# Kernel tuning notes

Measured on AMD Instinct MI355X. Metric: run time of the kernel, lower is better.

## Reference

```python
import jax, jax.numpy as jnp
import numpy as np

HEAD_DIM = 1024
SCALE = HEAD_DIM ** -0.25  # qk_scale defaults to exponent -0.25


def setup_inputs() -> dict:
    key = jax.random.key(0)
    ks = jax.random.split(key, 6)
    B_s, B_q, C = 4096, 4096, 1024
    return {
        "query": jax.random.normal(ks[0], (B_q, C), dtype=jnp.float32),
        "s": jax.random.normal(ks[1], (B_s, C), dtype=jnp.float32),
        "TG_prompt": jax.random.normal(ks[2], (B_s, C), dtype=jnp.float32),
        "W_qkv": jax.random.normal(ks[3], (3 * HEAD_DIM, C), dtype=jnp.float32) * (C ** -0.5),
        "W_proj_s": jax.random.normal(ks[4], (HEAD_DIM, HEAD_DIM), dtype=jnp.float32) * (HEAD_DIM ** -0.5),
        "W_proj_q": jax.random.normal(ks[5], (HEAD_DIM, HEAD_DIM), dtype=jnp.float32) * (HEAD_DIM ** -0.5),
    }


def reference(query, s, TG_prompt, W_qkv, W_proj_s, W_proj_q):
    B_s = s.shape[0]
    t = s + TG_prompt                       # [B_s, C]
    c = jnp.concatenate([t, query], axis=0)  # [B, C], B = B_s + B_q
    x = c @ W_qkv.T                          # [B, 3*head_dim]
    q, k, v = jnp.split(x, 3, axis=-1)       # each [B, head_dim]
    # separate sqrt-scale on q and k, then full [B, B] scores
    attn = jax.nn.softmax((q * SCALE) @ (k.T * SCALE), axis=-1)
    attn_cq = attn[:B_s, B_s:]               # [B_s, B_q]
    attn_qc = attn[B_s:, :B_s]               # [B_q, B_s]
    # matmul against raw query / s (NOT v), then per-branch projection
    x_s = (attn_cq @ query) @ W_proj_s.T     # [B_s, head_dim]
    x_q = (attn_qc @ s) @ W_proj_q.T         # [B_q, head_dim]
    return (x_s, x_q)
```

## Files before the change

### kernel.cpp

```cpp
#include <hip/hip_runtime.h>


typedef unsigned short u16;
typedef __bf16 bf16x8 __attribute__((ext_vector_type(8)));
typedef float f32x4 __attribute__((ext_vector_type(4)));
typedef unsigned short u16x8 __attribute__((ext_vector_type(8)));

#define DEVI static __device__ __forceinline__

DEVI u16 f2b(float f) {
  unsigned int u = __float_as_uint(f);
  u += 0x7fffu + ((u >> 16) & 1u);
  return (u16)(u >> 16);
}

DEVI float exp2_hw(float x) {
  float r;
  asm("v_exp_f32 %0, %1" : "=v"(r) : "v"(x));
  return r;
}

__global__ void prep_all(const float* __restrict__ query, const float* __restrict__ s,
                         const float* __restrict__ tg, const float* __restrict__ w0,
                         const float* __restrict__ w1, const float* __restrict__ w2,
                         u16* __restrict__ cB, u16* __restrict__ sBf,
                         u16* __restrict__ o0, u16* __restrict__ o1,
                         u16* __restrict__ o2, float* __restrict__ rowsum) {
  int b = blockIdx.x;
  if (b >= 6144) {
    int i = (b - 6144) * 1024 + (int)threadIdx.x * 4;
    rowsum[i] = 0.f; rowsum[i + 1] = 0.f; rowsum[i + 2] = 0.f; rowsum[i + 3] = 0.f;
    return;
  }
  if (b < 4096) {
    int base = (b * 256 + threadIdx.x) << 3;
    int row = base >> 10;
    u16x8 o;
    if (row < 4096) {
      float4 a0 = *(const float4*)(s + base);
      float4 a1 = *(const float4*)(s + base + 4);
      float4 b0 = *(const float4*)(tg + base);
      float4 b1 = *(const float4*)(tg + base + 4);
      u16x8 os;
      os[0] = f2b(a0.x); os[1] = f2b(a0.y); os[2] = f2b(a0.z); os[3] = f2b(a0.w);
      os[4] = f2b(a1.x); os[5] = f2b(a1.y); os[6] = f2b(a1.z); os[7] = f2b(a1.w);
      *(u16x8*)(sBf + base) = os;
      o[0] = f2b(a0.x + b0.x); o[1] = f2b(a0.y + b0.y);
      o[2] = f2b(a0.z + b0.z); o[3] = f2b(a0.w + b0.w);
      o[4] = f2b(a1.x + b1.x); o[5] = f2b(a1.y + b1.y);
      o[6] = f2b(a1.z + b1.z); o[7] = f2b(a1.w + b1.w);
    } else {
      int qb = base - 4096 * 1024;
      float4 a0 = *(const float4*)(query + qb);
      float4 a1 = *(const float4*)(query + qb + 4);
      o[0] = f2b(a0.x); o[1] = f2b(a0.y); o[2] = f2b(a0.z); o[3] = f2b(a0.w);
      o[4] = f2b(a1.x); o[5] = f2b(a1.y); o[6] = f2b(a1.z); o[7] = f2b(a1.w);
    }
    *(u16x8*)(cB + base) = o;
  } else {
    const float* in; u16* out; int lb;
    if (b < 5120)      { in = w0; out = o0; lb = b - 4096; }
    else if (b < 5632) { in = w1; out = o1; lb = b - 5120; }
    else               { in = w2; out = o2; lb = b - 5632; }
    int base = (lb * 256 + threadIdx.x) << 3;
    float4 a0 = *(const float4*)(in + base);
    float4 a1 = *(const float4*)(in + base + 4);
    u16x8 o;
    o[0] = f2b(a0.x); o[1] = f2b(a0.y); o[2] = f2b(a0.z); o[3] = f2b(a0.w);
    o[4] = f2b(a1.x); o[5] = f2b(a1.y); o[6] = f2b(a1.z); o[7] = f2b(a1.w);
    *(u16x8*)(out + base) = o;
  }
}

DEVI void kloop(const u16* Ab, const u16* Bb, int lda, int ldb, int K,
                u16* sA, u16* sB, int tid, int wr, int wc, f32x4 (&acc)[4][4]) {
  const int lane = tid & 63;
  const int ar = lane & 15;
  const int sr = tid >> 3;
  const int scL = (tid & 7) << 3;
  const int scG = ((tid & 7) ^ (sr & 7)) << 3;

  const int l7 = lane & 7, l16 = lane >> 4;
  const int p0b = (l16 ^ l7) << 4;
  const int offA0 = (wr + ar) * 128 + p0b;
  const int offB0 = (wc + ar) * 128 + p0b;
  const char* sAc = (const char*)sA;
  const char* sBc = (const char*)sB;

  for (int k0 = 0; k0 < K; k0 += 64) {
#pragma unroll
    for (int it = 0; it < 4; ++it) {
      int r = it * 64 + sr;
      __builtin_amdgcn_global_load_lds(
          (__attribute__((address_space(1))) void*)(Ab + (size_t)r * lda + k0 + scG),
          (__attribute__((address_space(3))) void*)(sA + r * 64 + scL), 16, 0, 0);
    }
#pragma unroll
    for (int it = 0; it < 2; ++it) {
      int r = it * 64 + sr;
      __builtin_amdgcn_global_load_lds(
          (__attribute__((address_space(1))) void*)(Bb + (size_t)r * ldb + k0 + scG),
          (__attribute__((address_space(3))) void*)(sB + r * 64 + scL), 16, 0, 0);
    }
    __syncthreads();
#pragma unroll
    for (int half = 0; half < 2; ++half) {
      const int px = half ? 64 : 0;
      bf16x8 af[4], bfr[4];
#pragma unroll
      for (int t = 0; t < 4; ++t)
        af[t] = *(const bf16x8*)(sAc + ((offA0 ^ px) + t * 2048));
#pragma unroll
      for (int t = 0; t < 4; ++t)
        bfr[t] = *(const bf16x8*)(sBc + ((offB0 ^ px) + t * 2048));
#pragma unroll
      for (int tm = 0; tm < 4; ++tm)
#pragma unroll
        for (int tn = 0; tn < 4; ++tn)
          acc[tm][tn] = __builtin_amdgcn_mfma_f32_16x16x32_bf16(
              af[tm], bfr[tn], acc[tm][tn], 0, 0, 0);
    }
    __syncthreads();
  }
}

__global__ __launch_bounds__(512)
void gemm_qkv(const u16* __restrict__ cB, const u16* __restrict__ WqkB,
              u16* __restrict__ qks,
              const u16* __restrict__ WpsB, const u16* __restrict__ WpqB,
              const u16* __restrict__ qBf, const u16* __restrict__ sBf,
              u16* __restrict__ VsT, u16* __restrict__ VqT,
              float sq, float sk) {
  __shared__ __align__(16) u16 sA[256 * 64];
  __shared__ __align__(16) u16 sB[128 * 64];
  const int b = blockIdx.x;
  const u16* Ap; const u16* Bp; u16* op;
  int bx, by, ldc;
  bool proj;
  if (b < 512) {
    proj = true;  bx = b & 15; by = b >> 4;
    Ap = cB; Bp = WqkB; op = qks; ldc = 2048;
  } else {
    proj = false;
    int b2 = b - 512;
    int z = b2 >> 7, rem = b2 & 127;
    bx = rem & 31; by = rem >> 5;
    Ap = z ? WpqB : WpsB; Bp = z ? sBf : qBf; op = z ? VqT : VsT; ldc = 4096;
  }
  const int tid = threadIdx.x;
  const int lane = tid & 63;
  const int wave = tid >> 6;
  const int wr = (wave >> 1) * 64;
  const int wc = (wave & 1) * 64;

  f32x4 acc[4][4];
#pragma unroll
  for (int i = 0; i < 4; ++i)
#pragma unroll
    for (int j = 0; j < 4; ++j) acc[i][j] = f32x4{0.f, 0.f, 0.f, 0.f};

  kloop(Ap + (size_t)(by * 256) * 1024, Bp + (size_t)(bx * 128) * 1024,
        1024, 1024, 1024, sA, sB, tid, wr, wc, acc);

  const int qr = (lane >> 4) * 4;
  const int qc = lane & 15;
#pragma unroll
  for (int tm = 0; tm < 4; ++tm)
#pragma unroll
    for (int r = 0; r < 4; ++r) {
      int row = by * 256 + wr + tm * 16 + qr + r;
#pragma unroll
      for (int tn = 0; tn < 4; ++tn) {
        int col = bx * 128 + wc + tn * 16 + qc;
        float sc = proj ? ((col < 1024) ? sq : sk) : 1.0f;
        op[(size_t)row * ldc + col] = f2b(acc[tm][tn][r] * sc);
      }
    }
}

__global__ __launch_bounds__(512)
void gemm_sc(const u16* __restrict__ A, const u16* __restrict__ B,
             u16* __restrict__ Pcq, u16* __restrict__ Pqc,
             float* __restrict__ rowsum) {
  __shared__ __align__(16) u16 lds[2][2][256 * 64];
  const int tid = threadIdx.x;
  const int lane = tid & 63;
  const int wave = tid >> 6;
  const int wm = wave >> 2;
  const int wn = wave & 3;
  const int bx = blockIdx.x, by = blockIdx.y;

  const int sr = tid >> 3;
  const int scL = (tid & 7) << 3;
  const int scG = ((tid & 7) ^ (sr & 7)) << 3;

  const int l7 = lane & 7, l16 = lane >> 4;
  const int ar = lane & 15;
  const int p0b = (l16 ^ l7) << 4;
  const int offA0 = (wm * 128 + ar) * 128 + p0b;
  const int offB0 = (wn * 64 + ar) * 128 + p0b;

  const u16* Ag = A + (size_t)(by * 256) * 2048;
  const u16* Bg = B + (size_t)(bx * 256) * 2048;

#define STAGE_SC(DST, K0)                                                     \
  _Pragma("unroll")                                                           \
  for (int it_ = 0; it_ < 4; ++it_) {                                         \
    const int r_ = it_ * 64 + sr;                                             \
    __builtin_amdgcn_global_load_lds(                                         \
        (__attribute__((address_space(1))) void*)(Ag + (size_t)r_ * 2048 + (K0) + scG), \
        (__attribute__((address_space(3))) void*)(&lds[DST][0][r_ * 64 + scL]), 16, 0, 0); \
    __builtin_amdgcn_global_load_lds(                                         \
        (__attribute__((address_space(1))) void*)(Bg + (size_t)r_ * 2048 + (K0) + scG), \
        (__attribute__((address_space(3))) void*)(&lds[DST][1][r_ * 64 + scL]), 16, 0, 0); \
  }

#define MFMA_Q(MQ, NQ)                                                        \
  _Pragma("unroll")                                                           \
  for (int tm_ = 0; tm_ < 4; ++tm_) {                                         \
    _Pragma("unroll")                                                         \
    for (int tn_ = 0; tn_ < 2; ++tn_) {                                       \
      _Pragma("unroll")                                                       \
      for (int kh_ = 0; kh_ < 2; ++kh_)                                       \
        acc[(MQ) * 4 + tm_][(NQ) * 2 + tn_] =                                 \
            __builtin_amdgcn_mfma_f32_16x16x32_bf16(                          \
                af[tm_][kh_], bfr[NQ][tn_][kh_],                              \
                acc[(MQ) * 4 + tm_][(NQ) * 2 + tn_], 0, 0, 0);                \
    }                                                                         \
  }

  f32x4 acc[8][4];
#pragma unroll
  for (int i = 0; i < 8; ++i)
#pragma unroll
    for (int j = 0; j < 4; ++j) acc[i][j] = f32x4{0.f, 0.f, 0.f, 0.f};

  STAGE_SC(0, 0)

#pragma unroll 1
  for (int kt = 0; kt < 16; ++kt) {
    const int cur = kt & 1;
    const char* sAc = (const char*)lds[cur][0];
    const char* sBc = (const char*)lds[cur][1];

    if (kt < 15) {
      STAGE_SC(cur ^ 1, (kt + 1) * 64)
      asm volatile("s_waitcnt vmcnt(8)\n\ts_barrier" ::: "memory");
    } else {
      asm volatile("s_waitcnt vmcnt(0)\n\ts_barrier" ::: "memory");
    }

    bf16x8 af[4][2];
    bf16x8 bfr[2][2][2];
#pragma unroll
    for (int t_ = 0; t_ < 4; ++t_) {
      af[t_][0] = *(const bf16x8*)(sAc + (offA0 + t_ * 2048));
      af[t_][1] = *(const bf16x8*)(sAc + ((offA0 + t_ * 2048) ^ 64));
    }
#pragma unroll
    for (int nq_ = 0; nq_ < 2; ++nq_)
#pragma unroll
      for (int t_ = 0; t_ < 2; ++t_) {
        bfr[nq_][t_][0] = *(const bf16x8*)(sBc + (offB0 + nq_ * 4096 + t_ * 2048));
        bfr[nq_][t_][1] = *(const bf16x8*)(sBc + ((offB0 + nq_ * 4096 + t_ * 2048) ^ 64));
      }
    asm volatile("s_waitcnt lgkmcnt(0)" ::: "memory");
    __builtin_amdgcn_sched_barrier(0);
    __builtin_amdgcn_s_setprio(1);
    MFMA_Q(0, 0)
    __builtin_amdgcn_s_setprio(0);
    asm volatile("s_barrier" ::: "memory");

    __builtin_amdgcn_s_setprio(1);
    MFMA_Q(0, 1)
    __builtin_amdgcn_s_setprio(0);
    asm volatile("s_barrier" ::: "memory");

#pragma unroll
    for (int t_ = 0; t_ < 4; ++t_) {
      af[t_][0] = *(const bf16x8*)(sAc + (offA0 + 8192 + t_ * 2048));
      af[t_][1] = *(const bf16x8*)(sAc + ((offA0 + 8192 + t_ * 2048) ^ 64));
    }
    asm volatile("s_waitcnt lgkmcnt(0)" ::: "memory");
    __builtin_amdgcn_sched_barrier(0);
    __builtin_amdgcn_s_setprio(1);
    MFMA_Q(1, 0)
    __builtin_amdgcn_s_setprio(0);
    asm volatile("s_barrier" ::: "memory");

    __builtin_amdgcn_s_setprio(1);
    MFMA_Q(1, 1)
    __builtin_amdgcn_s_setprio(0);
    asm volatile("s_barrier" ::: "memory");
  }

  const int qr = (lane >> 4) * 4;
  const int qc = lane & 15;
  const bool top = (by < 16);
  const bool left = (bx < 16);
  u16* pdst = nullptr;
  if (top && !left) pdst = Pcq;
  if (!top && left) pdst = Pqc;
  const int growb = by * 256 + wm * 128;
  const int rbase = growb - (top ? 0 : 4096);
  const int cbase = bx * 256 + wn * 64 - (left ? 0 : 4096);
#pragma unroll
  for (int i = 0; i < 8; ++i) {
    float e[4][4];
    float rsum[4] = {0.f, 0.f, 0.f, 0.f};
#pragma unroll
    for (int j = 0; j < 4; ++j)
#pragma unroll
      for (int r = 0; r < 4; ++r) {
        e[j][r] = exp2_hw(acc[i][j][r]);
        rsum[r] += e[j][r];
      }
#pragma unroll
    for (int r = 0; r < 4; ++r) {
      float v = rsum[r];
      v += __shfl_xor(v, 1);
      v += __shfl_xor(v, 2);
      v += __shfl_xor(v, 4);
      v += __shfl_xor(v, 8);
      if ((lane & 15) == 0)
        atomicAdd(&rowsum[growb + i * 16 + qr + r], v);
    }
    if (pdst) {
#pragma unroll
      for (int j = 0; j < 4; ++j)
#pragma unroll
        for (int r = 0; r < 4; ++r) {
          int row = rbase + i * 16 + qr + r;
          pdst[(size_t)row * 4096 + cbase + j * 16 + qc] = f2b(e[j][r]);
        }
    }
  }
#undef STAGE_SC
#undef MFMA_Q
}

template <int EPI>
__global__ __launch_bounds__(512)
void gemm_bt(const u16* __restrict__ A, const u16* __restrict__ A1,
             const u16* __restrict__ B, const u16* __restrict__ B1,
             int lda, int ldb, int K, int ldc,
             float* __restrict__ outf, float* __restrict__ outf1,
             const float* __restrict__ rs, const float* __restrict__ rs1,
             u16* __restrict__ Pcq, u16* __restrict__ Pqc,
             float* __restrict__ rowsum) {
  __shared__ __align__(16) u16 sA[256 * 64];
  __shared__ __align__(16) u16 sB[128 * 64];
  const int tid = threadIdx.x;
  const int lane = tid & 63;
  const int wave = tid >> 6;
  const int wr = (wave >> 1) * 64;
  const int wc = (wave & 1) * 64;
  const int by = blockIdx.y, bx = blockIdx.x;
  const int z = blockIdx.z;

  f32x4 acc[4][4];
#pragma unroll
  for (int i = 0; i < 4; ++i)
#pragma unroll
    for (int j = 0; j < 4; ++j) acc[i][j] = f32x4{0.f, 0.f, 0.f, 0.f};

  kloop((z ? A1 : A) + (size_t)(by * 256) * lda,
        (z ? B1 : B) + (size_t)(bx * 128) * ldb,
        lda, ldb, K, sA, sB, tid, wr, wc, acc);

  const int qr = (lane >> 4) * 4;
  const int qc = lane & 15;

  if constexpr (EPI == 4) {
    float* of = z ? outf1 : outf;
    const float* rsz = z ? rs1 : rs;
#pragma unroll
    for (int tm = 0; tm < 4; ++tm)
#pragma unroll
      for (int r = 0; r < 4; ++r) {
        int row = by * 256 + wr + tm * 16 + qr + r;
        float inv = 1.0f / rsz[row];
#pragma unroll
        for (int tn = 0; tn < 4; ++tn) {
          int col = bx * 128 + wc + tn * 16 + qc;
          of[(size_t)row * ldc + col] = acc[tm][tn][r] * inv;
        }
      }
  }
}


extern "C" void kernel_launch(void* const* d_in, const int* in_sizes, int n_in,
                              void* d_out, int out_size, void* d_ws, size_t ws_size,
                              hipStream_t stream) {
  (void)in_sizes; (void)n_in; (void)out_size; (void)ws_size;
  const float* query = (const float*)d_in[0];
  const float* s     = (const float*)d_in[1];
  const float* tg    = (const float*)d_in[2];
  const float* Wqkv  = (const float*)d_in[3];
  const float* Wps   = (const float*)d_in[4];
  const float* Wpq   = (const float*)d_in[5];
  float* out = (float*)d_out;

  char* ws = (char*)d_ws;
  u16* cB     = (u16*)ws; ws += (size_t)8192 * 1024 * 2;
  u16* sBf    = (u16*)ws; ws += (size_t)4096 * 1024 * 2;
  u16* qks    = (u16*)ws; ws += (size_t)8192 * 2048 * 2;
  u16* WqkB   = (u16*)ws; ws += (size_t)2048 * 1024 * 2;
  u16* WpsB   = (u16*)ws; ws += (size_t)1024 * 1024 * 2;
  u16* WpqB   = (u16*)ws; ws += (size_t)1024 * 1024 * 2;
  u16* VsT    = (u16*)ws; ws += (size_t)1024 * 4096 * 2;
  u16* VqT    = (u16*)ws; ws += (size_t)1024 * 4096 * 2;
  u16* Pcq    = (u16*)ws; ws += (size_t)4096 * 4096 * 2;
  u16* Pqc    = (u16*)ws; ws += (size_t)4096 * 4096 * 2;
  float* rowsum = (float*)ws;

  const u16* qBf = cB + (size_t)4096 * 1024;

  const float SCALE = 0.17677669529663687f;
  const float LOG2E = 1.4426950408889634f;

  prep_all<<<6152, 256, 0, stream>>>(query, s, tg, Wqkv, Wps, Wpq,
                                     cB, sBf, WqkB, WpsB, WpqB, rowsum);
  gemm_qkv<<<768, 512, 0, stream>>>(cB, WqkB, qks, WpsB, WpqB, qBf, sBf,
                                    VsT, VqT, SCALE * LOG2E, SCALE);
  gemm_sc<<<dim3(32, 32), 512, 0, stream>>>(qks, qks + 1024, Pcq, Pqc, rowsum);
  gemm_bt<4><<<dim3(8, 16, 2), 512, 0, stream>>>(
      Pcq, Pqc, VsT, VqT, 4096, 4096, 4096, 1024,
      out, out + (size_t)4096 * 1024, rowsum, rowsum + 4096,
      nullptr, nullptr, nullptr);
}
```

Before: 448.0 us.

## Deepen score GEMM pipeline to two-stage-ahead prefetch with staggered A/B reloads

Reworks the K loop of the score GEMM so the global-to-LDS loads for tile kt+2 are issued into the buffer being consumed, split into B and A halves. Each half is issued right after its last LDS read completes, instead of prefetching only one tile ahead at the top of the loop. Fragment loads are split into af0/af1/b0/b1 groups interleaved with the MFMA quarters, and the explicit lgkmcnt waits, sched barriers and one s_barrier per iteration are removed. The aim is to hide more global-load latency and cut synchronisation stalls. In exchange the buffer-reuse ordering becomes more fragile, and register pressure from extra fragment arrays may rise.

New measurement: 452.9 us. About the same (+1.1%).

```diff
diff --git a/kernel.cpp b/kernel.cpp
--- a/kernel.cpp
+++ b/kernel.cpp
@@ -203,29 +203,26 @@
   const u16* Ag = A + (size_t)(by * 256) * 2048;
   const u16* Bg = B + (size_t)(bx * 256) * 2048;
 
-#define STAGE_SC(DST, K0)                                                     \
+#define STG(BUF, MAT, HALF, K0, SRC)                                          \
   _Pragma("unroll")                                                           \
-  for (int it_ = 0; it_ < 4; ++it_) {                                         \
-    const int r_ = it_ * 64 + sr;                                             \
+  for (int l_ = 0; l_ < 2; ++l_) {                                            \
+    const int r_ = (HALF) * 128 + l_ * 64 + sr;                               \
     __builtin_amdgcn_global_load_lds(                                         \
-        (__attribute__((address_space(1))) void*)(Ag + (size_t)r_ * 2048 + (K0) + scG), \
-        (__attribute__((address_space(3))) void*)(&lds[DST][0][r_ * 64 + scL]), 16, 0, 0); \
-    __builtin_amdgcn_global_load_lds(                                         \
-        (__attribute__((address_space(1))) void*)(Bg + (size_t)r_ * 2048 + (K0) + scG), \
-        (__attribute__((address_space(3))) void*)(&lds[DST][1][r_ * 64 + scL]), 16, 0, 0); \
-  }
-
-#define MFMA_Q(MQ, NQ)                                                        \
+        (__attribute__((address_space(1))) void*)((SRC) + (size_t)r_ * 2048 + (K0) + scG), \
+        (__attribute__((address_space(3))) void*)(&lds[BUF][MAT][r_ * 64 + scL]), 16, 0, 0); \
+  }
+
+#define MFMA_Q(AF, BF, MB, NB)                                                \
   _Pragma("unroll")                                                           \
   for (int tm_ = 0; tm_ < 4; ++tm_) {                                         \
     _Pragma("unroll")                                                         \
     for (int tn_ = 0; tn_ < 2; ++tn_) {                                       \
       _Pragma("unroll")                                                       \
       for (int kh_ = 0; kh_ < 2; ++kh_)                                       \
-        acc[(MQ) * 4 + tm_][(NQ) * 2 + tn_] =                                 \
+        acc[(MB) + tm_][(NB) + tn_] =                                         \
             __builtin_amdgcn_mfma_f32_16x16x32_bf16(                          \
-                af[tm_][kh_], bfr[NQ][tn_][kh_],                              \
-                acc[(MQ) * 4 + tm_][(NQ) * 2 + tn_], 0, 0, 0);                \
+                AF[tm_][kh_], BF[tn_][kh_], acc[(MB) + tm_][(NB) + tn_],      \
+                0, 0, 0);                                                     \
     }                                                                         \
   }
 
@@ -235,7 +232,10 @@
 #pragma unroll
     for (int j = 0; j < 4; ++j) acc[i][j] = f32x4{0.f, 0.f, 0.f, 0.f};
 
-  STAGE_SC(0, 0)
+  STG(0, 0, 0, 0, Ag) STG(0, 0, 1, 0, Ag)
+  STG(0, 1, 0, 0, Bg) STG(0, 1, 1, 0, Bg)
+  STG(1, 0, 0, 64, Ag) STG(1, 0, 1, 64, Ag)
+  STG(1, 1, 0, 64, Bg) STG(1, 1, 1, 64, Bg)
 
 #pragma unroll 1
   for (int kt = 0; kt < 16; ++kt) {
@@ -243,55 +243,57 @@
     const char* sAc = (const char*)lds[cur][0];
     const char* sBc = (const char*)lds[cur][1];
 
-    if (kt < 15) {
-      STAGE_SC(cur ^ 1, (kt + 1) * 64)
+    if (kt < 15)
       asm volatile("s_waitcnt vmcnt(8)\n\ts_barrier" ::: "memory");
-    } else {
+    else
       asm volatile("s_waitcnt vmcnt(0)\n\ts_barrier" ::: "memory");
-    }
-
-    bf16x8 af[4][2];
-    bf16x8 bfr[2][2][2];
+
+    bf16x8 af0[4][2], af1[4][2], b0[2][2], b1[2][2];
 #pragma unroll
     for (int t_ = 0; t_ < 4; ++t_) {
-      af[t_][0] = *(const bf16x8*)(sAc + (offA0 + t_ * 2048));
-      af[t_][1] = *(const bf16x8*)(sAc + ((offA0 + t_ * 2048) ^ 64));
-    }
-#pragma unroll
-    for (int nq_ = 0; nq_ < 2; ++nq_)
-#pragma unroll
-      for (int t_ = 0; t_ < 2; ++t_) {
-        bfr[nq_][t_][0] = *(const bf16x8*)(sBc + (offB0 + nq_ * 4096 + t_ * 2048));
-        bfr[nq_][t_][1] = *(const bf16x8*)(sBc + ((offB0 + nq_ * 4096 + t_ * 2048) ^ 64));
-      }
-    asm volatile("s_waitcnt lgkmcnt(0)" ::: "memory");
-    __builtin_amdgcn_sched_barrier(0);
+      af0[t_][0] = *(const bf16x8*)(sAc + (offA0 + t_ * 2048));
+      af0[t_][1] = *(const bf16x8*)(sAc + ((offA0 + t_ * 2048) ^ 64));
+    }
+#pragma unroll
+    for (int t_ = 0; t_ < 2; ++t_) {
+      b0[t_][0] = *(const bf16x8*)(sBc + (offB0 + t_ * 2048));
+      b0[t_][1] = *(const bf16x8*)(sBc + ((offB0 + t_ * 2048) ^ 64));
+    }
     __builtin_amdgcn_s_setprio(1);
-    MFMA_Q(0, 0)
+    MFMA_Q(af0, b0, 0, 0)
+    __builtin_amdgcn_s_setprio(0);
+
+#pragma unroll
+    for (int t_ = 0; t_ < 2; ++t_) {
+      b1[t_][0] = *(const bf16x8*)(sBc + (offB0 + 4096 + t_ * 2048));
+      b1[t_][1] = *(const bf16x8*)(sBc + ((offB0 + 4096 + t_ * 2048) ^ 64));
+    }
+    __builtin_amdgcn_s_setprio(1);
+    MFMA_Q(af0, b1, 0, 2)
     __builtin_amdgcn_s_setprio(0);
     asm volatile("s_barrier" ::: "memory");
 
+    if (kt < 14) {
+      STG(cur, 1, 0, (kt + 2) * 64, Bg)
+      STG(cur, 1, 1, (kt + 2) * 64, Bg)
+    }
+#pragma unroll
+    for (int t_ = 0; t_ < 4; ++t_) {
+      af1[t_][0] = *(const bf16x8*)(sAc + (offA0 + 8192 + t_ * 2048));
+      af1[t_][1] = *(const bf16x8*)(sAc + ((offA0 + 8192 + t_ * 2048) ^ 64));
+    }
     __builtin_amdgcn_s_setprio(1);
-    MFMA_Q(0, 1)
+    MFMA_Q(af1, b0, 4, 0)
     __builtin_amdgcn_s_setprio(0);
     asm volatile("s_barrier" ::: "memory");
 
-#pragma unroll
-    for (int t_ = 0; t_ < 4; ++t_) {
-      af[t_][0] = *(const bf16x8*)(sAc + (offA0 + 8192 + t_ * 2048));
-      af[t_][1] = *(const bf16x8*)(sAc + ((offA0 + 8192 + t_ * 2048) ^ 64));
-    }
-    asm volatile("s_waitcnt lgkmcnt(0)" ::: "memory");
-    __builtin_amdgcn_sched_barrier(0);
+    if (kt < 14) {
+      STG(cur, 0, 0, (kt + 2) * 64, Ag)
+      STG(cur, 0, 1, (kt + 2) * 64, Ag)
+    }
     __builtin_amdgcn_s_setprio(1);
-    MFMA_Q(1, 0)
+    MFMA_Q(af1, b1, 4, 2)
     __builtin_amdgcn_s_setprio(0);
-    asm volatile("s_barrier" ::: "memory");
-
-    __builtin_amdgcn_s_setprio(1);
-    MFMA_Q(1, 1)
-    __builtin_amdgcn_s_setprio(0);
-    asm volatile("s_barrier" ::: "memory");
   }
 
   const int qr = (lane >> 4) * 4;
@@ -335,7 +337,7 @@
         }
     }
   }
-#undef STAGE_SC
+#undef STG
 #undef MFMA_Q
 }
 
```
